# Kernel tuning notes

Hardware: AMD Instinct MI355X
Metric: run time of the kernel (lower is better)

The kernel has to match this reference:

```python
import jax, jax.numpy as jnp
import numpy as np


def setup_inputs() -> dict:
    key = jax.random.key(0)
    k1, k2 = jax.random.split(key)
    n, B = 64, 256
    return {
        "out_matrix": jax.random.normal(k1, (n, n, B), dtype=jnp.float32),
        "label_matrix": jax.random.normal(k2, (n, n, B), dtype=jnp.float32),
        "margin": jnp.ones((), dtype=jnp.float32),
        "sample_num": 64,
    }


def reference(out_matrix, label_matrix, margin, sample_num):
    # out_matrix, label_matrix: [n, n, B]; sample_num == n (rows fully used).
    out = jnp.transpose(out_matrix, (2, 0, 1))   # [B, n, n]
    lab = jnp.transpose(label_matrix, (2, 0, 1))  # [B, n, n]
    # Per batch slice, per row r: pairwise diffs d[j,k] = out[r,j]-out[r,k]
    d = out[..., :, None] - out[..., None, :]     # [B, n, n, n]
    l = lab[..., :, None] - lab[..., None, :]     # [B, n, n, n]
    # Hinge: relu(margin - d*l), summed over everything (diagonal contributes margin,
    # matching the original which includes j==k terms).
    loss = jnp.sum(jax.nn.relu(margin - d * l))
    # flat_accuracy per batch slice: argmax over dim 1 of the [n,n] slice,
    # i.e. axis=2 of the [B,n,n] layout (torch argmax(preds,1) on squeezed slice).
    correction_num = jnp.sum(jnp.argmax(out, axis=2) == jnp.argmax(lab, axis=2))
    return loss, correction_num
```

## Files before the change

### kernel.cpp

```cpp
#include <hip/hip_runtime.h>
#include <math.h>

constexpr int N = 64;
constexpr int B = 256;
constexpr int BCHUNK = 64;
constexpr int JG = 8;
constexpr int THREADS = 512;

__global__ void init_out_kernel(float* out) {
    out[0] = 0.0f;
    out[1] = 0.0f;
}

__global__ __launch_bounds__(THREADS)
void pm_hinge_kernel(const float* __restrict__ outm,
                     const float* __restrict__ labm,
                     const float* __restrict__ margin,
                     float* __restrict__ dout)
{
    __shared__ float o_s[N * BCHUNK];
    __shared__ float l_s[N * BCHUNK];
    __shared__ float wsum[THREADS / 64];

    const int r  = blockIdx.x;
    const int b0 = blockIdx.y * BCHUNK;
    const int t  = threadIdx.x;

    const float* src_o = outm + (size_t)r * (N * B) + b0;
    const float* src_l = labm + (size_t)r * (N * B) + b0;
#pragma unroll
    for (int f = t; f < (N * BCHUNK) / 4; f += THREADS) {
        const int j  = f >> 4;
        const int b4 = (f & 15) * 4;
        const float4 vo = *(const float4*)(src_o + j * B + b4);
        const float4 vl = *(const float4*)(src_l + j * B + b4);
        *(float4*)(&o_s[j * BCHUNK + b4]) = vo;
        *(float4*)(&l_s[j * BCHUNK + b4]) = vl;
    }
    __syncthreads();

    const float m  = margin[0];
    const int   b  = t & 63;
    const int   jg = t >> 6;

    float oj[JG], lj[JG];
#pragma unroll
    for (int i = 0; i < JG; ++i) {
        oj[i] = o_s[(jg * JG + i) * BCHUNK + b];
        lj[i] = l_s[(jg * JG + i) * BCHUNK + b];
    }

    float acc = 0.0f;
#pragma unroll 4
    for (int k = 0; k < N; ++k) {
        const float ok = o_s[k * BCHUNK + b];
        const float lk = l_s[k * BCHUNK + b];
#pragma unroll
        for (int i = 0; i < JG; ++i) {
            const float d    = oj[i] - ok;
            const float dl   = lj[i] - lk;
            const float term = fmaf(-d, dl, m);
            acc += fmaxf(term, 0.0f);
        }
    }

    if (t < 64) {
        const int bb = t;
        float bo = o_s[bb]; int io = 0;
        float bl = l_s[bb]; int il = 0;
#pragma unroll 4
        for (int j = 1; j < N; ++j) {
            const float vo = o_s[j * BCHUNK + bb];
            if (vo > bo) { bo = vo; io = j; }
            const float vl = l_s[j * BCHUNK + bb];
            if (vl > bl) { bl = vl; il = j; }
        }
        const unsigned long long mask = __ballot(io == il);
        if (bb == 0) atomicAdd(dout + 1, (float)__popcll(mask));
    }

#pragma unroll
    for (int off = 32; off > 0; off >>= 1)
        acc += __shfl_down(acc, off, 64);
    if (b == 0) wsum[jg] = acc;
    __syncthreads();
    if (t == 0) {
        float s = 0.0f;
#pragma unroll
        for (int w = 0; w < THREADS / 64; ++w) s += wsum[w];
        atomicAdd(dout, s);
    }
}

extern "C" void kernel_launch(void* const* d_in, const int* in_sizes, int n_in,
                              void* d_out, int out_size, void* d_ws, size_t ws_size,
                              hipStream_t stream) {
    const float* outm   = (const float*)d_in[0];
    const float* labm   = (const float*)d_in[1];
    const float* margin = (const float*)d_in[2];
    float* out = (float*)d_out;

    init_out_kernel<<<1, 1, 0, stream>>>(out);
    pm_hinge_kernel<<<dim3(N, B / BCHUNK), THREADS, 0, stream>>>(outm, labm, margin, out);
}
```

Measured before the change: 78.20 us.

## Exploit pair symmetry in hinge loss and replace atomics with two-pass reduction

Result: faster. 68.66 us (-12.2%).

```diff
diff --git a/kernel.cpp b/kernel.cpp
--- a/kernel.cpp
+++ b/kernel.cpp
@@ -1,30 +1,29 @@
 #include <hip/hip_runtime.h>
 #include <math.h>
+
 
 constexpr int N = 64;
 constexpr int B = 256;
 constexpr int BCHUNK = 64;
-constexpr int JG = 8;
-constexpr int THREADS = 512;
-
-__global__ void init_out_kernel(float* out) {
-    out[0] = 0.0f;
-    out[1] = 0.0f;
-}
+constexpr int NJG = 16;
+constexpr int JI = 4;
+constexpr int THREADS = BCHUNK * NJG;
+constexpr int NBLK = N * (B / BCHUNK);
 
 __global__ __launch_bounds__(THREADS)
-void pm_hinge_kernel(const float* __restrict__ outm,
-                     const float* __restrict__ labm,
-                     const float* __restrict__ margin,
-                     float* __restrict__ dout)
+void pm_hinge_partial(const float* __restrict__ outm,
+                      const float* __restrict__ labm,
+                      const float* __restrict__ margin,
+                      float* __restrict__ ws)
 {
     __shared__ float o_s[N * BCHUNK];
     __shared__ float l_s[N * BCHUNK];
-    __shared__ float wsum[THREADS / 64];
+    __shared__ float wsum[NJG];
 
-    const int r  = blockIdx.x;
-    const int b0 = blockIdx.y * BCHUNK;
-    const int t  = threadIdx.x;
+    const int r   = blockIdx.x;
+    const int b0  = blockIdx.y * BCHUNK;
+    const int t   = threadIdx.x;
+    const int blk = blockIdx.y * N + r;
 
     const float* src_o = outm + (size_t)r * (N * B) + b0;
     const float* src_l = labm + (size_t)r * (N * B) + b0;
@@ -32,10 +31,8 @@
     for (int f = t; f < (N * BCHUNK) / 4; f += THREADS) {
         const int j  = f >> 4;
         const int b4 = (f & 15) * 4;
-        const float4 vo = *(const float4*)(src_o + j * B + b4);
-        const float4 vl = *(const float4*)(src_l + j * B + b4);
-        *(float4*)(&o_s[j * BCHUNK + b4]) = vo;
-        *(float4*)(&l_s[j * BCHUNK + b4]) = vl;
+        *(float4*)(&o_s[j * BCHUNK + b4]) = *(const float4*)(src_o + j * B + b4);
+        *(float4*)(&l_s[j * BCHUNK + b4]) = *(const float4*)(src_l + j * B + b4);
     }
     __syncthreads();
 
@@ -43,27 +40,40 @@
     const int   b  = t & 63;
     const int   jg = t >> 6;
 
-    float oj[JG], lj[JG];
+    float oj[JI], lj[JI];
 #pragma unroll
-    for (int i = 0; i < JG; ++i) {
-        oj[i] = o_s[(jg * JG + i) * BCHUNK + b];
-        lj[i] = l_s[(jg * JG + i) * BCHUNK + b];
+    for (int i = 0; i < JI; ++i) {
+        oj[i] = o_s[(jg + NJG * i) * BCHUNK + b];
+        lj[i] = l_s[(jg + NJG * i) * BCHUNK + b];
     }
 
     float acc = 0.0f;
+
+#define TERM(i) acc += fmaxf(fmaf(-(oj[i] - ok), lj[i] - lk, m), 0.0f)
+
 #pragma unroll 4
-    for (int k = 0; k < N; ++k) {
-        const float ok = o_s[k * BCHUNK + b];
-        const float lk = l_s[k * BCHUNK + b];
-#pragma unroll
-        for (int i = 0; i < JG; ++i) {
-            const float d    = oj[i] - ok;
-            const float dl   = lj[i] - lk;
-            const float term = fmaf(-d, dl, m);
-            acc += fmaxf(term, 0.0f);
-        }
+    for (int k = jg + 1; k <= jg + 16; ++k) {
+        const float ok = o_s[k * BCHUNK + b], lk = l_s[k * BCHUNK + b];
+        TERM(0);
     }
+#pragma unroll 4
+    for (int k = jg + 17; k <= jg + 32; ++k) {
+        const float ok = o_s[k * BCHUNK + b], lk = l_s[k * BCHUNK + b];
+        TERM(0); TERM(1);
+    }
+#pragma unroll 4
+    for (int k = jg + 33; k <= jg + 48; ++k) {
+        const float ok = o_s[k * BCHUNK + b], lk = l_s[k * BCHUNK + b];
+        TERM(0); TERM(1); TERM(2);
+    }
+#pragma unroll 2
+    for (int k = jg + 49; k < N; ++k) {
+        const float ok = o_s[k * BCHUNK + b], lk = l_s[k * BCHUNK + b];
+        TERM(0); TERM(1); TERM(2); TERM(3);
+    }
+#undef TERM
 
+    float cnt = 0.0f;
     if (t < 64) {
         const int bb = t;
         float bo = o_s[bb]; int io = 0;
@@ -76,7 +86,7 @@
             if (vl > bl) { bl = vl; il = j; }
         }
         const unsigned long long mask = __ballot(io == il);
-        if (bb == 0) atomicAdd(dout + 1, (float)__popcll(mask));
+        cnt = (float)__popcll(mask);
     }
 
 #pragma unroll
@@ -87,8 +97,33 @@
     if (t == 0) {
         float s = 0.0f;
 #pragma unroll
-        for (int w = 0; w < THREADS / 64; ++w) s += wsum[w];
-        atomicAdd(dout, s);
+        for (int w = 0; w < NJG; ++w) s += wsum[w];
+        ws[blk] = s;
+        ws[NBLK + blk] = cnt;
+    }
+}
+
+__global__ __launch_bounds__(64)
+void pm_hinge_reduce(const float* __restrict__ ws,
+                     const float* __restrict__ margin,
+                     float* __restrict__ dout)
+{
+    const int t = threadIdx.x;
+    float s = 0.0f, c = 0.0f;
+#pragma unroll
+    for (int i = 0; i < NBLK / 64; ++i) {
+        s += ws[t + 64 * i];
+        c += ws[NBLK + t + 64 * i];
+    }
+#pragma unroll
+    for (int off = 32; off > 0; off >>= 1) {
+        s += __shfl_down(s, off, 64);
+        c += __shfl_down(c, off, 64);
+    }
+    if (t == 0) {
+        const float m = margin[0];
+        dout[0] = 2.0f * s + (float)(N * (size_t)N * B) * fmaxf(m, 0.0f);
+        dout[1] = c;
     }
 }
 
@@ -99,7 +134,8 @@
     const float* labm   = (const float*)d_in[1];
     const float* margin = (const float*)d_in[2];
     float* out = (float*)d_out;
+    float* ws  = (float*)d_ws;
 
-    init_out_kernel<<<1, 1, 0, stream>>>(out);
-    pm_hinge_kernel<<<dim3(N, B / BCHUNK), THREADS, 0, stream>>>(outm, labm, margin, out);
+    pm_hinge_partial<<<dim3(N, B / BCHUNK), THREADS, 0, stream>>>(outm, labm, margin, ws);
+    pm_hinge_reduce<<<1, 64, 0, stream>>>(ws, margin, out);
 }
```
